# Performance work log

Measured on AMD Instinct MI355X. Metric: run time of the kernel, lower is better.

The kernel has to match this reference:

```python
import jax, jax.numpy as jnp
import numpy as np

N_NODES = 50000
N_EDGES = 800000
IN_DIM = 4
HID = 64
N_LAYERS = 3
BN_EPS = 1e-5


def setup_inputs() -> dict:
    key = jax.random.key(0)
    ks = jax.random.split(key, 16)
    x = jax.random.normal(ks[0], (N_NODES, IN_DIM), dtype=jnp.float32)
    edge_index = jax.random.randint(ks[1], (2, N_EDGES), 0, N_NODES, dtype=jnp.int32)
    # input projection
    W_in = jax.random.normal(ks[2], (IN_DIM, HID), dtype=jnp.float32) * 0.1
    b_in = jnp.zeros((HID,), dtype=jnp.float32)
    # stacked per-layer GCN weights and BatchNorm (eval-mode) params
    conv_w = jax.random.normal(ks[3], (N_LAYERS, HID, HID), dtype=jnp.float32) * 0.1
    conv_b = jnp.zeros((N_LAYERS, HID), dtype=jnp.float32)
    bn_gamma = jnp.ones((N_LAYERS, HID), dtype=jnp.float32)
    bn_beta = jnp.zeros((N_LAYERS, HID), dtype=jnp.float32)
    bn_mean = jax.random.normal(ks[4], (N_LAYERS, HID), dtype=jnp.float32) * 0.01
    bn_var = jnp.abs(jax.random.normal(ks[5], (N_LAYERS, HID), dtype=jnp.float32)) * 0.1 + 1.0
    # output projection: Linear(HID,HID) -> ReLU -> Dropout(eval: identity) -> Linear(HID,OUT)
    W1 = jax.random.normal(ks[6], (HID, HID), dtype=jnp.float32) * 0.1
    b1 = jnp.zeros((HID,), dtype=jnp.float32)
    W2 = jax.random.normal(ks[7], (HID, IN_DIM), dtype=jnp.float32) * 0.01  # xavier gain 0.1
    b2 = jnp.zeros((IN_DIM,), dtype=jnp.float32)
    return {
        "x": x, "edge_index": edge_index,
        "W_in": W_in, "b_in": b_in,
        "conv_w": conv_w, "conv_b": conv_b,
        "bn_gamma": bn_gamma, "bn_beta": bn_beta,
        "bn_mean": bn_mean, "bn_var": bn_var,
        "W1": W1, "b1": b1, "W2": W2, "b2": b2,
    }


def _gcn_graph(edge_index, n_nodes):
    """Add self loops and compute symmetric GCN normalization per edge."""
    loops = jnp.arange(n_nodes, dtype=edge_index.dtype)
    src = jnp.concatenate([edge_index[0], loops])
    dst = jnp.concatenate([edge_index[1], loops])
    deg = jax.ops.segment_sum(jnp.ones_like(dst, dtype=jnp.float32), dst,
                              num_segments=n_nodes)  # in-degree incl. self loop
    dinv = jax.lax.rsqrt(jnp.maximum(deg, 1e-12))
    enorm = dinv[src] * dinv[dst]  # [E+N]
    return src, dst, enorm


def reference(x, edge_index, W_in, b_in, conv_w, conv_b, bn_gamma, bn_beta,
              bn_mean, bn_var, W1, b1, W2, b2):
    n = x.shape[0]
    src, dst, enorm = _gcn_graph(edge_index, n)

    input_x = x
    h = x @ W_in + b_in  # [N, HID]
    for i in range(N_LAYERS):
        residual = h
        # GCNConv: linear -> normalized gather/scatter aggregate -> bias
        hw = h @ conv_w[i]
        msg = hw[src] * enorm[:, None]  # [E+N, HID] irregular gather
        h = jax.ops.segment_sum(msg, dst, num_segments=n) + conv_b[i]
        # BatchNorm1d (eval) + ReLU (dropout is identity in eval)
        h = (h - bn_mean[i]) * jax.lax.rsqrt(bn_var[i] + BN_EPS) * bn_gamma[i] + bn_beta[i]
        h = jax.nn.relu(h)
        h = h + residual  # shapes always match (HID == HID)
    # output projection MLP
    delta = jax.nn.relu(h @ W1 + b1) @ W2 + b2  # [N, IN_DIM]
    return input_x + delta
```

## Files before the change

### kernel.cpp

```cpp
#include <hip/hip_runtime.h>

#define HID 64
#define CAP 64

__device__ __forceinline__ float bf2f(unsigned short u) {
    return __uint_as_float(((unsigned)u) << 16);
}
__device__ __forceinline__ unsigned short f2bf(float f) {
    unsigned u = __float_as_uint(f);
    u += 0x7FFF + ((u >> 16) & 1);
    return (unsigned short)(u >> 16);
}

__global__ void fill_gemm(const int* __restrict__ eidx, int* __restrict__ cursor,
                          int* __restrict__ col, int E, int n, int nodes_per,
                          int chunk, int fillBlocks,
                          const float* __restrict__ x, const float* __restrict__ Win,
                          const float* __restrict__ bin, const float* __restrict__ W,
                          float* __restrict__ h, unsigned short* __restrict__ hws0) {
    if (blockIdx.x < fillBlocks) {
        int p = blockIdx.x & 7;
        int q = blockIdx.x >> 3;
        const int* __restrict__ dst = eidx + E;
        int lo = p * nodes_per;
        int hi = lo + nodes_per;
        int beg = q * chunk;
        int end = min(beg + chunk, E);
        int vend = beg + ((end - beg) & ~3);
        for (int e = beg + threadIdx.x * 4; e < vend; e += 1024) {
            int4 dv = *(const int4*)&dst[e];
            if (dv.x >= lo && dv.x < hi) {
                int s = eidx[e];
                int pos = atomicAdd(&cursor[dv.x], 1);
                if (pos < CAP) col[(dv.x << 6) + pos] = s;
            }
            if (dv.y >= lo && dv.y < hi) {
                int s = eidx[e + 1];
                int pos = atomicAdd(&cursor[dv.y], 1);
                if (pos < CAP) col[(dv.y << 6) + pos] = s;
            }
            if (dv.z >= lo && dv.z < hi) {
                int s = eidx[e + 2];
                int pos = atomicAdd(&cursor[dv.z], 1);
                if (pos < CAP) col[(dv.z << 6) + pos] = s;
            }
            if (dv.w >= lo && dv.w < hi) {
                int s = eidx[e + 3];
                int pos = atomicAdd(&cursor[dv.w], 1);
                if (pos < CAP) col[(dv.w << 6) + pos] = s;
            }
        }
        for (int e = vend + threadIdx.x; e < end; e += 256) {
            int d = dst[e];
            if (d >= lo && d < hi) {
                int s = eidx[e];
                int pos = atomicAdd(&cursor[d], 1);
                if (pos < CAP) col[(d << 6) + pos] = s;
            }
        }
        return;
    }
    __shared__ float wl[64 * 64];
    __shared__ float winl[256];
    __shared__ float binl[64];
    __shared__ float hl[256];
    int b = blockIdx.x - fillBlocks;
    int tid = threadIdx.x;
#pragma unroll
    for (int i = 0; i < 16; ++i) wl[tid + 256 * i] = W[tid + 256 * i];
    winl[tid] = Win[tid];
    if (tid < 64) binl[tid] = bin[tid];
    int j = tid & 63;
    int w = tid >> 6;
    for (int c = 0; c < 8; ++c) {
        int v = b * 32 + c * 4 + w;
        __syncthreads();
        float hv = 0.f;
        if (v < n) {
            float4 xv = *(const float4*)&x[(size_t)v * 4];
            hv = binl[j] + xv.x * winl[j] + xv.y * winl[64 + j]
                         + xv.z * winl[128 + j] + xv.w * winl[192 + j];
            h[(size_t)v * 64 + j] = hv;
        }
        hl[tid] = hv;
        __syncthreads();
        if (v < n) {
            const float* hr = &hl[w * 64];
            float acc = 0.f;
#pragma unroll
            for (int k = 0; k < 64; ++k) acc += hr[k] * wl[k * 64 + j];
            hws0[(size_t)v * 64 + j] = f2bf(acc);
        }
    }
}

#define GATHER_BODY(hws4, col, cursor, beg, end, s0, s1, s2, s3, gl)              \
    {                                                                             \
        int e = beg;                                                              \
        for (; e + 7 < end; e += 8) {                                             \
            int c0 = col[e], c1 = col[e+1], c2 = col[e+2], c3 = col[e+3];         \
            int c4 = col[e+4], c5 = col[e+5], c6 = col[e+6], c7 = col[e+7];       \
            float d0 = rsqrtf((float)cursor[c0] + 1.0f);                          \
            float d1 = rsqrtf((float)cursor[c1] + 1.0f);                          \
            float d2 = rsqrtf((float)cursor[c2] + 1.0f);                          \
            float d3 = rsqrtf((float)cursor[c3] + 1.0f);                          \
            float d4 = rsqrtf((float)cursor[c4] + 1.0f);                          \
            float d5 = rsqrtf((float)cursor[c5] + 1.0f);                          \
            float d6 = rsqrtf((float)cursor[c6] + 1.0f);                          \
            float d7 = rsqrtf((float)cursor[c7] + 1.0f);                          \
            ushort4 m0 = hws4[(size_t)c0 * 16 + gl];                              \
            ushort4 m1 = hws4[(size_t)c1 * 16 + gl];                              \
            ushort4 m2 = hws4[(size_t)c2 * 16 + gl];                              \
            ushort4 m3 = hws4[(size_t)c3 * 16 + gl];                              \
            ushort4 m4 = hws4[(size_t)c4 * 16 + gl];                              \
            ushort4 m5 = hws4[(size_t)c5 * 16 + gl];                              \
            ushort4 m6 = hws4[(size_t)c6 * 16 + gl];                              \
            ushort4 m7 = hws4[(size_t)c7 * 16 + gl];                              \
            s0 = fmaf(bf2f(m0.x), d0, s0); s0 = fmaf(bf2f(m1.x), d1, s0);         \
            s0 = fmaf(bf2f(m2.x), d2, s0); s0 = fmaf(bf2f(m3.x), d3, s0);         \
            s0 = fmaf(bf2f(m4.x), d4, s0); s0 = fmaf(bf2f(m5.x), d5, s0);         \
            s0 = fmaf(bf2f(m6.x), d6, s0); s0 = fmaf(bf2f(m7.x), d7, s0);         \
            s1 = fmaf(bf2f(m0.y), d0, s1); s1 = fmaf(bf2f(m1.y), d1, s1);         \
            s1 = fmaf(bf2f(m2.y), d2, s1); s1 = fmaf(bf2f(m3.y), d3, s1);         \
            s1 = fmaf(bf2f(m4.y), d4, s1); s1 = fmaf(bf2f(m5.y), d5, s1);         \
            s1 = fmaf(bf2f(m6.y), d6, s1); s1 = fmaf(bf2f(m7.y), d7, s1);         \
            s2 = fmaf(bf2f(m0.z), d0, s2); s2 = fmaf(bf2f(m1.z), d1, s2);         \
            s2 = fmaf(bf2f(m2.z), d2, s2); s2 = fmaf(bf2f(m3.z), d3, s2);         \
            s2 = fmaf(bf2f(m4.z), d4, s2); s2 = fmaf(bf2f(m5.z), d5, s2);         \
            s2 = fmaf(bf2f(m6.z), d6, s2); s2 = fmaf(bf2f(m7.z), d7, s2);         \
            s3 = fmaf(bf2f(m0.w), d0, s3); s3 = fmaf(bf2f(m1.w), d1, s3);         \
            s3 = fmaf(bf2f(m2.w), d2, s3); s3 = fmaf(bf2f(m3.w), d3, s3);         \
            s3 = fmaf(bf2f(m4.w), d4, s3); s3 = fmaf(bf2f(m5.w), d5, s3);         \
            s3 = fmaf(bf2f(m6.w), d6, s3); s3 = fmaf(bf2f(m7.w), d7, s3);         \
        }                                                                         \
        for (; e + 3 < end; e += 4) {                                             \
            int c0 = col[e], c1 = col[e+1], c2 = col[e+2], c3 = col[e+3];         \
            float d0 = rsqrtf((float)cursor[c0] + 1.0f);                          \
            float d1 = rsqrtf((float)cursor[c1] + 1.0f);                          \
            float d2 = rsqrtf((float)cursor[c2] + 1.0f);                          \
            float d3 = rsqrtf((float)cursor[c3] + 1.0f);                          \
            ushort4 m0 = hws4[(size_t)c0 * 16 + gl];                              \
            ushort4 m1 = hws4[(size_t)c1 * 16 + gl];                              \
            ushort4 m2 = hws4[(size_t)c2 * 16 + gl];                              \
            ushort4 m3 = hws4[(size_t)c3 * 16 + gl];                              \
            s0 = fmaf(bf2f(m0.x), d0, s0); s0 = fmaf(bf2f(m1.x), d1, s0);         \
            s0 = fmaf(bf2f(m2.x), d2, s0); s0 = fmaf(bf2f(m3.x), d3, s0);         \
            s1 = fmaf(bf2f(m0.y), d0, s1); s1 = fmaf(bf2f(m1.y), d1, s1);         \
            s1 = fmaf(bf2f(m2.y), d2, s1); s1 = fmaf(bf2f(m3.y), d3, s1);         \
            s2 = fmaf(bf2f(m0.z), d0, s2); s2 = fmaf(bf2f(m1.z), d1, s2);         \
            s2 = fmaf(bf2f(m2.z), d2, s2); s2 = fmaf(bf2f(m3.z), d3, s2);         \
            s3 = fmaf(bf2f(m0.w), d0, s3); s3 = fmaf(bf2f(m1.w), d1, s3);         \
            s3 = fmaf(bf2f(m2.w), d2, s3); s3 = fmaf(bf2f(m3.w), d3, s3);         \
        }                                                                         \
        for (; e < end; ++e) {                                                    \
            int c0 = col[e];                                                      \
            float d0 = rsqrtf((float)cursor[c0] + 1.0f);                          \
            ushort4 me = hws4[(size_t)c0 * 16 + gl];                              \
            s0 = fmaf(bf2f(me.x), d0, s0); s1 = fmaf(bf2f(me.y), d0, s1);         \
            s2 = fmaf(bf2f(me.z), d0, s2); s3 = fmaf(bf2f(me.w), d0, s3);         \
        }                                                                         \
    }

__global__ void gather_gemm(const int* __restrict__ cursor, const int* __restrict__ col,
                            const unsigned short* __restrict__ hws_in,
                            float* __restrict__ h,
                            const float* __restrict__ cb, const float* __restrict__ gamma,
                            const float* __restrict__ beta, const float* __restrict__ mean,
                            const float* __restrict__ var, const float* __restrict__ Wn,
                            unsigned short* __restrict__ hws_out, int n) {
    __shared__ float wl[64 * 64];
    __shared__ float hl[16 * 64];
    int tid = threadIdx.x;
#pragma unroll
    for (int i = 0; i < 16; ++i) wl[tid + 256 * i] = Wn[tid + 256 * i];
    int lane = tid & 63, wave = tid >> 6;
    int grp = lane >> 4, gl = lane & 15;
    int ln = wave * 4 + grp;
    int v = blockIdx.x * 16 + ln;
    bool valid = v < n;
    int vv = valid ? v : 0;
    int j0 = gl * 4;
    const ushort4* hws4 = (const ushort4*)hws_in;
    int cnt = cursor[vv];
    float di = rsqrtf((float)cnt + 1.0f);
    ushort4 m = hws4[(size_t)vv * 16 + gl];
    float s0 = bf2f(m.x) * di, s1 = bf2f(m.y) * di,
          s2 = bf2f(m.z) * di, s3 = bf2f(m.w) * di;
    int beg = vv << 6;
    int end = beg + (valid ? min(cnt, CAP) : 0);
    GATHER_BODY(hws4, col, cursor, beg, end, s0, s1, s2, s3, gl)
    float4 cbv = *(const float4*)&cb[j0];
    float4 mnv = *(const float4*)&mean[j0];
    float4 vrv = *(const float4*)&var[j0];
    float4 gmv = *(const float4*)&gamma[j0];
    float4 btv = *(const float4*)&beta[j0];
    float4 hres = *(const float4*)&h[(size_t)vv * 64 + j0];
    float4 o;
    o.x = fmaxf((s0 * di + cbv.x - mnv.x) * rsqrtf(vrv.x + 1e-5f) * gmv.x + btv.x, 0.f) + hres.x;
    o.y = fmaxf((s1 * di + cbv.y - mnv.y) * rsqrtf(vrv.y + 1e-5f) * gmv.y + btv.y, 0.f) + hres.y;
    o.z = fmaxf((s2 * di + cbv.z - mnv.z) * rsqrtf(vrv.z + 1e-5f) * gmv.z + btv.z, 0.f) + hres.z;
    o.w = fmaxf((s3 * di + cbv.w - mnv.w) * rsqrtf(vrv.w + 1e-5f) * gmv.w + btv.w, 0.f) + hres.w;
    if (valid) *(float4*)&h[(size_t)vv * 64 + j0] = o;
    *(float4*)&hl[ln * 64 + j0] = o;
    __syncthreads();
    int j = lane;
    for (int c = 0; c < 4; ++c) {
        int ln2 = wave * 4 + c;
        int v2 = blockIdx.x * 16 + ln2;
        if (v2 < n) {
            const float* hr = &hl[ln2 * 64];
            float acc = 0.f;
#pragma unroll
            for (int k = 0; k < 64; ++k) acc += hr[k] * wl[k * 64 + j];
            hws_out[(size_t)v2 * 64 + j] = f2bf(acc);
        }
    }
}

__global__ void gather_mlp(const int* __restrict__ cursor, const int* __restrict__ col,
                           const unsigned short* __restrict__ hws_in,
                           const float* __restrict__ h,
                           const float* __restrict__ cb, const float* __restrict__ gamma,
                           const float* __restrict__ beta, const float* __restrict__ mean,
                           const float* __restrict__ var, const float* __restrict__ x,
                           const float* __restrict__ W1, const float* __restrict__ b1,
                           const float* __restrict__ W2, const float* __restrict__ b2,
                           float* __restrict__ out, int n) {
    __shared__ float wl[64 * 64];
    __shared__ float w2l[256];
    __shared__ float hl[16 * 64];
    __shared__ float tl[16 * 68];
    int tid = threadIdx.x;
#pragma unroll
    for (int i = 0; i < 16; ++i) wl[tid + 256 * i] = W1[tid + 256 * i];
    w2l[tid] = W2[tid];
    int lane = tid & 63, wave = tid >> 6;
    int grp = lane >> 4, gl = lane & 15;
    int ln = wave * 4 + grp;
    int v = blockIdx.x * 16 + ln;
    bool valid = v < n;
    int vv = valid ? v : 0;
    int j0 = gl * 4;
    const ushort4* hws4 = (const ushort4*)hws_in;
    int cnt = cursor[vv];
    float di = rsqrtf((float)cnt + 1.0f);
    ushort4 m = hws4[(size_t)vv * 16 + gl];
    float s0 = bf2f(m.x) * di, s1 = bf2f(m.y) * di,
          s2 = bf2f(m.z) * di, s3 = bf2f(m.w) * di;
    int beg = vv << 6;
    int end = beg + (valid ? min(cnt, CAP) : 0);
    GATHER_BODY(hws4, col, cursor, beg, end, s0, s1, s2, s3, gl)
    float4 cbv = *(const float4*)&cb[j0];
    float4 mnv = *(const float4*)&mean[j0];
    float4 vrv = *(const float4*)&var[j0];
    float4 gmv = *(const float4*)&gamma[j0];
    float4 btv = *(const float4*)&beta[j0];
    float4 hres = *(const float4*)&h[(size_t)vv * 64 + j0];
    float4 o;
    o.x = fmaxf((s0 * di + cbv.x - mnv.x) * rsqrtf(vrv.x + 1e-5f) * gmv.x + btv.x, 0.f) + hres.x;
    o.y = fmaxf((s1 * di + cbv.y - mnv.y) * rsqrtf(vrv.y + 1e-5f) * gmv.y + btv.y, 0.f) + hres.y;
    o.z = fmaxf((s2 * di + cbv.z - mnv.z) * rsqrtf(vrv.z + 1e-5f) * gmv.z + btv.z, 0.f) + hres.z;
    o.w = fmaxf((s3 * di + cbv.w - mnv.w) * rsqrtf(vrv.w + 1e-5f) * gmv.w + btv.w, 0.f) + hres.w;
    *(float4*)&hl[ln * 64 + j0] = o;
    __syncthreads();
    int j = lane;
    float b1j = b1[j];
    for (int c = 0; c < 4; ++c) {
        int ln2 = wave * 4 + c;
        const float* hr = &hl[ln2 * 64];
        float acc = b1j;
#pragma unroll
        for (int k = 0; k < 64; ++k) acc += hr[k] * wl[k * 64 + j];
        tl[ln2 * 68 + j] = fmaxf(acc, 0.f);
    }
    __syncthreads();
    if (tid < 64) {
        int ln2 = tid >> 2, mm = tid & 3;
        int v2 = blockIdx.x * 16 + ln2;
        if (v2 < n) {
            const float* tr = &tl[ln2 * 68];
            float acc = b2[mm];
#pragma unroll
            for (int k = 0; k < 64; ++k) acc += tr[k] * w2l[k * 4 + mm];
            out[(size_t)v2 * 4 + mm] = x[(size_t)v2 * 4 + mm] + acc;
        }
    }
}

extern "C" void kernel_launch(void* const* d_in, const int* in_sizes, int n_in,
                              void* d_out, int out_size, void* d_ws, size_t ws_size,
                              hipStream_t stream) {
    const float* x     = (const float*)d_in[0];
    const int*   eidx  = (const int*)  d_in[1];
    const float* Win   = (const float*)d_in[2];
    const float* bin   = (const float*)d_in[3];
    const float* convw = (const float*)d_in[4];
    const float* convb = (const float*)d_in[5];
    const float* gamma = (const float*)d_in[6];
    const float* beta  = (const float*)d_in[7];
    const float* mean  = (const float*)d_in[8];
    const float* var   = (const float*)d_in[9];
    const float* W1    = (const float*)d_in[10];
    const float* b1    = (const float*)d_in[11];
    const float* W2    = (const float*)d_in[12];
    const float* b2    = (const float*)d_in[13];
    float* out = (float*)d_out;

    int n = in_sizes[0] / 4;
    int E = in_sizes[1] / 2;
    const int B = 256;

    char* p = (char*)d_ws;
    size_t nh = (size_t)n * 64;
    float*          h      = (float*)p;          p += nh * 4;
    unsigned short* hws0   = (unsigned short*)p; p += nh * 2;
    unsigned short* hws1   = (unsigned short*)p; p += nh * 2;
    int*            cursor = (int*)p;            p += ((size_t)n + 16) * 4;
    int*            col    = (int*)p;            p += (size_t)n * CAP * 4;

    const int GP = 128;
    int fillBlocks = GP * 8;
    int nodes_per = (n + 7) / 8;
    int chunk = (((E + GP - 1) / GP) + 3) & ~3;

    hipMemsetAsync(cursor, 0, (size_t)n * 4, stream);
    int NB32 = (n + 31) / 32;
    fill_gemm<<<fillBlocks + NB32, B, 0, stream>>>(
        eidx, cursor, col, E, n, nodes_per, chunk, fillBlocks,
        x, Win, bin, convw, h, hws0);

    int NB16 = (n + 15) / 16;
    gather_gemm<<<NB16, B, 0, stream>>>(cursor, col, hws0, h,
        convb, gamma, beta, mean, var, convw + 4096, hws1, n);
    gather_gemm<<<NB16, B, 0, stream>>>(cursor, col, hws1, h,
        convb + 64, gamma + 64, beta + 64, mean + 64, var + 64, convw + 8192, hws0, n);
    gather_mlp<<<NB16, B, 0, stream>>>(cursor, col, hws0, h,
        convb + 128, gamma + 128, beta + 128, mean + 128, var + 128,
        x, W1, b1, W2, b2, out, n);
}
```

Baseline: 233.2 us.

## Partition each node's neighbor list by source half using packed dual counters

The per-node cursor now packs two 16-bit counters, one for sources below n/2 and one for sources above. Low-half sources are stored from the front of the 64-slot list and high-half sources from the back. The gather then runs two passes, low-index sources first and high-index sources second, aiming for better cache locality on the irregular hws reads. This adds a second loop with its own remainder handling and extra decode ALU, and the degree is now capped per half rather than overall.

```diff
diff --git a/kernel.cpp b/kernel.cpp
--- a/kernel.cpp
+++ b/kernel.cpp
@@ -12,8 +12,10 @@
     return (unsigned short)(u >> 16);
 }
 
-__global__ void fill_gemm(const int* __restrict__ eidx, int* __restrict__ cursor,
-                          int* __restrict__ col, int E, int n, int nodes_per,
+#define DINV(cc) rsqrtf((float)(((cc) & 0xffffu) + ((cc) >> 16)) + 1.0f)
+
+__global__ void fill_gemm(const int* __restrict__ eidx, unsigned* __restrict__ cursor,
+                          int* __restrict__ col, int E, int n, int mid, int nodes_per,
                           int chunk, int fillBlocks,
                           const float* __restrict__ x, const float* __restrict__ Win,
                           const float* __restrict__ bin, const float* __restrict__ W,
@@ -29,34 +31,23 @@
         int vend = beg + ((end - beg) & ~3);
         for (int e = beg + threadIdx.x * 4; e < vend; e += 1024) {
             int4 dv = *(const int4*)&dst[e];
-            if (dv.x >= lo && dv.x < hi) {
-                int s = eidx[e];
-                int pos = atomicAdd(&cursor[dv.x], 1);
-                if (pos < CAP) col[(dv.x << 6) + pos] = s;
+#define FILL_ONE(d, ei)                                                        \
+            if (d >= lo && d < hi) {                                           \
+                int s = eidx[ei];                                              \
+                bool low = s < mid;                                            \
+                unsigned old = atomicAdd(&cursor[d], low ? 1u : 0x10000u);     \
+                unsigned cp = low ? (old & 0xffffu) : (old >> 16);             \
+                if (cp < CAP) col[(d << 6) + (low ? cp : (CAP - 1u - cp))] = s;\
             }
-            if (dv.y >= lo && dv.y < hi) {
-                int s = eidx[e + 1];
-                int pos = atomicAdd(&cursor[dv.y], 1);
-                if (pos < CAP) col[(dv.y << 6) + pos] = s;
-            }
-            if (dv.z >= lo && dv.z < hi) {
-                int s = eidx[e + 2];
-                int pos = atomicAdd(&cursor[dv.z], 1);
-                if (pos < CAP) col[(dv.z << 6) + pos] = s;
-            }
-            if (dv.w >= lo && dv.w < hi) {
-                int s = eidx[e + 3];
-                int pos = atomicAdd(&cursor[dv.w], 1);
-                if (pos < CAP) col[(dv.w << 6) + pos] = s;
-            }
+            FILL_ONE(dv.x, e)
+            FILL_ONE(dv.y, e + 1)
+            FILL_ONE(dv.z, e + 2)
+            FILL_ONE(dv.w, e + 3)
         }
         for (int e = vend + threadIdx.x; e < end; e += 256) {
             int d = dst[e];
-            if (d >= lo && d < hi) {
-                int s = eidx[e];
-                int pos = atomicAdd(&cursor[d], 1);
-                if (pos < CAP) col[(d << 6) + pos] = s;
-            }
+            FILL_ONE(d, e)
+#undef FILL_ONE
         }
         return;
     }
@@ -94,20 +85,16 @@
     }
 }
 
-#define GATHER_BODY(hws4, col, cursor, beg, end, s0, s1, s2, s3, gl)              \
+#define GATHER_BODY(hws4, col, cur, beg, end, s0, s1, s2, s3, gl)                 \
     {                                                                             \
         int e = beg;                                                              \
         for (; e + 7 < end; e += 8) {                                             \
             int c0 = col[e], c1 = col[e+1], c2 = col[e+2], c3 = col[e+3];         \
             int c4 = col[e+4], c5 = col[e+5], c6 = col[e+6], c7 = col[e+7];       \
-            float d0 = rsqrtf((float)cursor[c0] + 1.0f);                          \
-            float d1 = rsqrtf((float)cursor[c1] + 1.0f);                          \
-            float d2 = rsqrtf((float)cursor[c2] + 1.0f);                          \
-            float d3 = rsqrtf((float)cursor[c3] + 1.0f);                          \
-            float d4 = rsqrtf((float)cursor[c4] + 1.0f);                          \
-            float d5 = rsqrtf((float)cursor[c5] + 1.0f);                          \
-            float d6 = rsqrtf((float)cursor[c6] + 1.0f);                          \
-            float d7 = rsqrtf((float)cursor[c7] + 1.0f);                          \
+            unsigned k0 = cur[c0], k1 = cur[c1], k2 = cur[c2], k3 = cur[c3];      \
+            unsigned k4 = cur[c4], k5 = cur[c5], k6 = cur[c6], k7 = cur[c7];      \
+            float d0 = DINV(k0), d1 = DINV(k1), d2 = DINV(k2), d3 = DINV(k3);     \
+            float d4 = DINV(k4), d5 = DINV(k5), d6 = DINV(k6), d7 = DINV(k7);     \
             ushort4 m0 = hws4[(size_t)c0 * 16 + gl];                              \
             ushort4 m1 = hws4[(size_t)c1 * 16 + gl];                              \
             ushort4 m2 = hws4[(size_t)c2 * 16 + gl];                              \
@@ -135,10 +122,8 @@
         }                                                                         \
         for (; e + 3 < end; e += 4) {                                             \
             int c0 = col[e], c1 = col[e+1], c2 = col[e+2], c3 = col[e+3];         \
-            float d0 = rsqrtf((float)cursor[c0] + 1.0f);                          \
-            float d1 = rsqrtf((float)cursor[c1] + 1.0f);                          \
-            float d2 = rsqrtf((float)cursor[c2] + 1.0f);                          \
-            float d3 = rsqrtf((float)cursor[c3] + 1.0f);                          \
+            unsigned k0 = cur[c0], k1 = cur[c1], k2 = cur[c2], k3 = cur[c3];      \
+            float d0 = DINV(k0), d1 = DINV(k1), d2 = DINV(k2), d3 = DINV(k3);     \
             ushort4 m0 = hws4[(size_t)c0 * 16 + gl];                              \
             ushort4 m1 = hws4[(size_t)c1 * 16 + gl];                              \
             ushort4 m2 = hws4[(size_t)c2 * 16 + gl];                              \
@@ -154,14 +139,15 @@
         }                                                                         \
         for (; e < end; ++e) {                                                    \
             int c0 = col[e];                                                      \
-            float d0 = rsqrtf((float)cursor[c0] + 1.0f);                          \
+            unsigned k0 = cur[c0];                                                \
+            float d0 = DINV(k0);                                                  \
             ushort4 me = hws4[(size_t)c0 * 16 + gl];                              \
             s0 = fmaf(bf2f(me.x), d0, s0); s1 = fmaf(bf2f(me.y), d0, s1);         \
             s2 = fmaf(bf2f(me.z), d0, s2); s3 = fmaf(bf2f(me.w), d0, s3);         \
         }                                                                         \
     }
 
-__global__ void gather_gemm(const int* __restrict__ cursor, const int* __restrict__ col,
+__global__ void gather_gemm(const unsigned* __restrict__ cursor, const int* __restrict__ col,
                             const unsigned short* __restrict__ hws_in,
                             float* __restrict__ h,
                             const float* __restrict__ cb, const float* __restrict__ gamma,
@@ -181,14 +167,17 @@
     int vv = valid ? v : 0;
     int j0 = gl * 4;
     const ushort4* hws4 = (const ushort4*)hws_in;
-    int cnt = cursor[vv];
-    float di = rsqrtf((float)cnt + 1.0f);
+    unsigned cc = cursor[vv];
+    int nlo = cc & 0xffffu, nhi = cc >> 16;
+    float di = rsqrtf((float)(nlo + nhi) + 1.0f);
     ushort4 m = hws4[(size_t)vv * 16 + gl];
     float s0 = bf2f(m.x) * di, s1 = bf2f(m.y) * di,
           s2 = bf2f(m.z) * di, s3 = bf2f(m.w) * di;
-    int beg = vv << 6;
-    int end = beg + (valid ? min(cnt, CAP) : 0);
-    GATHER_BODY(hws4, col, cursor, beg, end, s0, s1, s2, s3, gl)
+    int base = vv << 6;
+    int nlo_c = valid ? min(nlo, CAP) : 0;
+    int nhi_c = valid ? min(nhi, CAP) : 0;
+    GATHER_BODY(hws4, col, cursor, base, base + nlo_c, s0, s1, s2, s3, gl)
+    GATHER_BODY(hws4, col, cursor, base + CAP - nhi_c, base + CAP, s0, s1, s2, s3, gl)
     float4 cbv = *(const float4*)&cb[j0];
     float4 mnv = *(const float4*)&mean[j0];
     float4 vrv = *(const float4*)&var[j0];
@@ -217,7 +206,7 @@
     }
 }
 
-__global__ void gather_mlp(const int* __restrict__ cursor, const int* __restrict__ col,
+__global__ void gather_mlp(const unsigned* __restrict__ cursor, const int* __restrict__ col,
                            const unsigned short* __restrict__ hws_in,
                            const float* __restrict__ h,
                            const float* __restrict__ cb, const float* __restrict__ gamma,
@@ -242,14 +231,17 @@
     int vv = valid ? v : 0;
     int j0 = gl * 4;
     const ushort4* hws4 = (const ushort4*)hws_in;
-    int cnt = cursor[vv];
-    float di = rsqrtf((float)cnt + 1.0f);
+    unsigned cc = cursor[vv];
+    int nlo = cc & 0xffffu, nhi = cc >> 16;
+    float di = rsqrtf((float)(nlo + nhi) + 1.0f);
     ushort4 m = hws4[(size_t)vv * 16 + gl];
     float s0 = bf2f(m.x) * di, s1 = bf2f(m.y) * di,
           s2 = bf2f(m.z) * di, s3 = bf2f(m.w) * di;
-    int beg = vv << 6;
-    int end = beg + (valid ? min(cnt, CAP) : 0);
-    GATHER_BODY(hws4, col, cursor, beg, end, s0, s1, s2, s3, gl)
+    int base = vv << 6;
+    int nlo_c = valid ? min(nlo, CAP) : 0;
+    int nhi_c = valid ? min(nhi, CAP) : 0;
+    GATHER_BODY(hws4, col, cursor, base, base + nlo_c, s0, s1, s2, s3, gl)
+    GATHER_BODY(hws4, col, cursor, base + CAP - nhi_c, base + CAP, s0, s1, s2, s3, gl)
     float4 cbv = *(const float4*)&cb[j0];
     float4 mnv = *(const float4*)&mean[j0];
     float4 vrv = *(const float4*)&var[j0];
@@ -315,18 +307,19 @@
     float*          h      = (float*)p;          p += nh * 4;
     unsigned short* hws0   = (unsigned short*)p; p += nh * 2;
     unsigned short* hws1   = (unsigned short*)p; p += nh * 2;
-    int*            cursor = (int*)p;            p += ((size_t)n + 16) * 4;
+    unsigned*       cursor = (unsigned*)p;       p += ((size_t)n + 16) * 4;
     int*            col    = (int*)p;            p += (size_t)n * CAP * 4;
 
     const int GP = 128;
     int fillBlocks = GP * 8;
     int nodes_per = (n + 7) / 8;
     int chunk = (((E + GP - 1) / GP) + 3) & ~3;
+    int mid = n >> 1;
 
     hipMemsetAsync(cursor, 0, (size_t)n * 4, stream);
     int NB32 = (n + 31) / 32;
     fill_gemm<<<fillBlocks + NB32, B, 0, stream>>>(
-        eidx, cursor, col, E, n, nodes_per, chunk, fillBlocks,
+        eidx, cursor, col, E, n, mid, nodes_per, chunk, fillBlocks,
         x, Win, bin, convw, h, hws0);
 
     int NB16 = (n + 15) / 16;
```

Measured after the change: 250.9 us. +7.6%, slower.

## Prescale GCN features by source degree and widen gather to 8 bf16 per lane

Applied to the files above, without the earlier changes.

The GEMM epilogues of the first two gather kernels now multiply each output row by its own rsqrt(deg), so later layers can sum neighbour rows without looking up each neighbour's degree. This removes a dependent cursor load and an rsqrt per edge in layers two and three. Each lane now loads 8 bf16 values (16 bytes), and a block handles 32 nodes instead of 16. The cost is more shared memory per block and more registers per thread, which may lower occupancy, and the first layer still uses the per-edge degree path because fill_gemm writes unscaled features.

```diff
diff --git a/kernel.cpp b/kernel.cpp
--- a/kernel.cpp
+++ b/kernel.cpp
@@ -1,7 +1,8 @@
 #include <hip/hip_runtime.h>
 
-#define HID 64
 #define CAP 64
+
+typedef unsigned short us8 __attribute__((ext_vector_type(8)));
 
 __device__ __forceinline__ float bf2f(unsigned short u) {
     return __uint_as_float(((unsigned)u) << 16);
@@ -94,73 +95,60 @@
     }
 }
 
-#define GATHER_BODY(hws4, col, cursor, beg, end, s0, s1, s2, s3, gl)              \
+#define GH_D8(hwsp, col, cur, beg, end, s, gl8)                                   \
     {                                                                             \
         int e = beg;                                                              \
         for (; e + 7 < end; e += 8) {                                             \
-            int c0 = col[e], c1 = col[e+1], c2 = col[e+2], c3 = col[e+3];         \
-            int c4 = col[e+4], c5 = col[e+5], c6 = col[e+6], c7 = col[e+7];       \
-            float d0 = rsqrtf((float)cursor[c0] + 1.0f);                          \
-            float d1 = rsqrtf((float)cursor[c1] + 1.0f);                          \
-            float d2 = rsqrtf((float)cursor[c2] + 1.0f);                          \
-            float d3 = rsqrtf((float)cursor[c3] + 1.0f);                          \
-            float d4 = rsqrtf((float)cursor[c4] + 1.0f);                          \
-            float d5 = rsqrtf((float)cursor[c5] + 1.0f);                          \
-            float d6 = rsqrtf((float)cursor[c6] + 1.0f);                          \
-            float d7 = rsqrtf((float)cursor[c7] + 1.0f);                          \
-            ushort4 m0 = hws4[(size_t)c0 * 16 + gl];                              \
-            ushort4 m1 = hws4[(size_t)c1 * 16 + gl];                              \
-            ushort4 m2 = hws4[(size_t)c2 * 16 + gl];                              \
-            ushort4 m3 = hws4[(size_t)c3 * 16 + gl];                              \
-            ushort4 m4 = hws4[(size_t)c4 * 16 + gl];                              \
-            ushort4 m5 = hws4[(size_t)c5 * 16 + gl];                              \
-            ushort4 m6 = hws4[(size_t)c6 * 16 + gl];                              \
-            ushort4 m7 = hws4[(size_t)c7 * 16 + gl];                              \
-            s0 = fmaf(bf2f(m0.x), d0, s0); s0 = fmaf(bf2f(m1.x), d1, s0);         \
-            s0 = fmaf(bf2f(m2.x), d2, s0); s0 = fmaf(bf2f(m3.x), d3, s0);         \
-            s0 = fmaf(bf2f(m4.x), d4, s0); s0 = fmaf(bf2f(m5.x), d5, s0);         \
-            s0 = fmaf(bf2f(m6.x), d6, s0); s0 = fmaf(bf2f(m7.x), d7, s0);         \
-            s1 = fmaf(bf2f(m0.y), d0, s1); s1 = fmaf(bf2f(m1.y), d1, s1);         \
-            s1 = fmaf(bf2f(m2.y), d2, s1); s1 = fmaf(bf2f(m3.y), d3, s1);         \
-            s1 = fmaf(bf2f(m4.y), d4, s1); s1 = fmaf(bf2f(m5.y), d5, s1);         \
-            s1 = fmaf(bf2f(m6.y), d6, s1); s1 = fmaf(bf2f(m7.y), d7, s1);         \
-            s2 = fmaf(bf2f(m0.z), d0, s2); s2 = fmaf(bf2f(m1.z), d1, s2);         \
-            s2 = fmaf(bf2f(m2.z), d2, s2); s2 = fmaf(bf2f(m3.z), d3, s2);         \
-            s2 = fmaf(bf2f(m4.z), d4, s2); s2 = fmaf(bf2f(m5.z), d5, s2);         \
-            s2 = fmaf(bf2f(m6.z), d6, s2); s2 = fmaf(bf2f(m7.z), d7, s2);         \
-            s3 = fmaf(bf2f(m0.w), d0, s3); s3 = fmaf(bf2f(m1.w), d1, s3);         \
-            s3 = fmaf(bf2f(m2.w), d2, s3); s3 = fmaf(bf2f(m3.w), d3, s3);         \
-            s3 = fmaf(bf2f(m4.w), d4, s3); s3 = fmaf(bf2f(m5.w), d5, s3);         \
-            s3 = fmaf(bf2f(m6.w), d6, s3); s3 = fmaf(bf2f(m7.w), d7, s3);         \
-        }                                                                         \
-        for (; e + 3 < end; e += 4) {                                             \
-            int c0 = col[e], c1 = col[e+1], c2 = col[e+2], c3 = col[e+3];         \
-            float d0 = rsqrtf((float)cursor[c0] + 1.0f);                          \
-            float d1 = rsqrtf((float)cursor[c1] + 1.0f);                          \
-            float d2 = rsqrtf((float)cursor[c2] + 1.0f);                          \
-            float d3 = rsqrtf((float)cursor[c3] + 1.0f);                          \
-            ushort4 m0 = hws4[(size_t)c0 * 16 + gl];                              \
-            ushort4 m1 = hws4[(size_t)c1 * 16 + gl];                              \
-            ushort4 m2 = hws4[(size_t)c2 * 16 + gl];                              \
-            ushort4 m3 = hws4[(size_t)c3 * 16 + gl];                              \
-            s0 = fmaf(bf2f(m0.x), d0, s0); s0 = fmaf(bf2f(m1.x), d1, s0);         \
-            s0 = fmaf(bf2f(m2.x), d2, s0); s0 = fmaf(bf2f(m3.x), d3, s0);         \
-            s1 = fmaf(bf2f(m0.y), d0, s1); s1 = fmaf(bf2f(m1.y), d1, s1);         \
-            s1 = fmaf(bf2f(m2.y), d2, s1); s1 = fmaf(bf2f(m3.y), d3, s1);         \
-            s2 = fmaf(bf2f(m0.z), d0, s2); s2 = fmaf(bf2f(m1.z), d1, s2);         \
-            s2 = fmaf(bf2f(m2.z), d2, s2); s2 = fmaf(bf2f(m3.z), d3, s2);         \
-            s3 = fmaf(bf2f(m0.w), d0, s3); s3 = fmaf(bf2f(m1.w), d1, s3);         \
-            s3 = fmaf(bf2f(m2.w), d2, s3); s3 = fmaf(bf2f(m3.w), d3, s3);         \
+            int cc[8]; float dd[8]; us8 mm[8];                                    \
+            _Pragma("unroll")                                                     \
+            for (int i = 0; i < 8; ++i) cc[i] = col[e + i];                       \
+            _Pragma("unroll")                                                     \
+            for (int i = 0; i < 8; ++i)                                           \
+                mm[i] = *(const us8*)&hwsp[(size_t)cc[i] * 64 + (gl8) * 8];       \
+            _Pragma("unroll")                                                     \
+            for (int i = 0; i < 8; ++i)                                           \
+                dd[i] = rsqrtf((float)cur[cc[i]] + 1.0f);                         \
+            _Pragma("unroll")                                                     \
+            for (int i = 0; i < 8; ++i) {                                         \
+                _Pragma("unroll")                                                 \
+                for (int f = 0; f < 8; ++f)                                       \
+                    s[f] = fmaf(bf2f(mm[i][f]), dd[i], s[f]);                     \
+            }                                                                     \
         }                                                                         \
         for (; e < end; ++e) {                                                    \
             int c0 = col[e];                                                      \
-            float d0 = rsqrtf((float)cursor[c0] + 1.0f);                          \
-            ushort4 me = hws4[(size_t)c0 * 16 + gl];                              \
-            s0 = fmaf(bf2f(me.x), d0, s0); s1 = fmaf(bf2f(me.y), d0, s1);         \
-            s2 = fmaf(bf2f(me.z), d0, s2); s3 = fmaf(bf2f(me.w), d0, s3);         \
+            float d0 = rsqrtf((float)cur[c0] + 1.0f);                             \
+            us8 me = *(const us8*)&hwsp[(size_t)c0 * 64 + (gl8) * 8];             \
+            _Pragma("unroll")                                                     \
+            for (int f = 0; f < 8; ++f)                                           \
+                s[f] = fmaf(bf2f(me[f]), d0, s[f]);                               \
         }                                                                         \
     }
 
+#define GH_P8(hwsp, col, beg, end, s, gl8)                                        \
+    {                                                                             \
+        int e = beg;                                                              \
+        for (; e + 7 < end; e += 8) {                                             \
+            int cc[8]; us8 mm[8];                                                 \
+            _Pragma("unroll")                                                     \
+            for (int i = 0; i < 8; ++i) cc[i] = col[e + i];                       \
+            _Pragma("unroll")                                                     \
+            for (int i = 0; i < 8; ++i)                                           \
+                mm[i] = *(const us8*)&hwsp[(size_t)cc[i] * 64 + (gl8) * 8];       \
+            _Pragma("unroll")                                                     \
+            for (int f = 0; f < 8; ++f)                                           \
+                s[f] += bf2f(mm[0][f]) + bf2f(mm[1][f]) + bf2f(mm[2][f])          \
+                      + bf2f(mm[3][f]) + bf2f(mm[4][f]) + bf2f(mm[5][f])          \
+                      + bf2f(mm[6][f]) + bf2f(mm[7][f]);                          \
+        }                                                                         \
+        for (; e < end; ++e) {                                                    \
+            us8 me = *(const us8*)&hwsp[(size_t)col[e] * 64 + (gl8) * 8];         \
+            _Pragma("unroll")                                                     \
+            for (int f = 0; f < 8; ++f) s[f] += bf2f(me[f]);                      \
+        }                                                                         \
+    }
+
+template <bool PRESCALED>
 __global__ void gather_gemm(const int* __restrict__ cursor, const int* __restrict__ col,
                             const unsigned short* __restrict__ hws_in,
                             float* __restrict__ h,
@@ -169,50 +157,62 @@
                             const float* __restrict__ var, const float* __restrict__ Wn,
                             unsigned short* __restrict__ hws_out, int n) {
     __shared__ float wl[64 * 64];
-    __shared__ float hl[16 * 64];
+    __shared__ float hl[32 * 64];
     int tid = threadIdx.x;
 #pragma unroll
     for (int i = 0; i < 16; ++i) wl[tid + 256 * i] = Wn[tid + 256 * i];
     int lane = tid & 63, wave = tid >> 6;
-    int grp = lane >> 4, gl = lane & 15;
-    int ln = wave * 4 + grp;
-    int v = blockIdx.x * 16 + ln;
+    int grp8 = lane >> 3, gl8 = lane & 7;
+    int ln = wave * 8 + grp8;
+    int v = blockIdx.x * 32 + ln;
     bool valid = v < n;
     int vv = valid ? v : 0;
-    int j0 = gl * 4;
-    const ushort4* hws4 = (const ushort4*)hws_in;
     int cnt = cursor[vv];
     float di = rsqrtf((float)cnt + 1.0f);
-    ushort4 m = hws4[(size_t)vv * 16 + gl];
-    float s0 = bf2f(m.x) * di, s1 = bf2f(m.y) * di,
-          s2 = bf2f(m.z) * di, s3 = bf2f(m.w) * di;
+    us8 m = *(const us8*)&hws_in[(size_t)vv * 64 + gl8 * 8];
+    float s[8];
+#pragma unroll
+    for (int f = 0; f < 8; ++f) s[f] = PRESCALED ? bf2f(m[f]) : bf2f(m[f]) * di;
     int beg = vv << 6;
     int end = beg + (valid ? min(cnt, CAP) : 0);
-    GATHER_BODY(hws4, col, cursor, beg, end, s0, s1, s2, s3, gl)
-    float4 cbv = *(const float4*)&cb[j0];
-    float4 mnv = *(const float4*)&mean[j0];
-    float4 vrv = *(const float4*)&var[j0];
-    float4 gmv = *(const float4*)&gamma[j0];
-    float4 btv = *(const float4*)&beta[j0];
-    float4 hres = *(const float4*)&h[(size_t)vv * 64 + j0];
-    float4 o;
-    o.x = fmaxf((s0 * di + cbv.x - mnv.x) * rsqrtf(vrv.x + 1e-5f) * gmv.x + btv.x, 0.f) + hres.x;
-    o.y = fmaxf((s1 * di + cbv.y - mnv.y) * rsqrtf(vrv.y + 1e-5f) * gmv.y + btv.y, 0.f) + hres.y;
-    o.z = fmaxf((s2 * di + cbv.z - mnv.z) * rsqrtf(vrv.z + 1e-5f) * gmv.z + btv.z, 0.f) + hres.z;
-    o.w = fmaxf((s3 * di + cbv.w - mnv.w) * rsqrtf(vrv.w + 1e-5f) * gmv.w + btv.w, 0.f) + hres.w;
-    if (valid) *(float4*)&h[(size_t)vv * 64 + j0] = o;
-    *(float4*)&hl[ln * 64 + j0] = o;
+    if (PRESCALED) {
+        GH_P8(hws_in, col, beg, end, s, gl8)
+    } else {
+        GH_D8(hws_in, col, cursor, beg, end, s, gl8)
+    }
+    int j0 = gl8 * 8;
+    float o[8];
+#pragma unroll
+    for (int hf = 0; hf < 2; ++hf) {
+        int jb = j0 + hf * 4;
+        float4 cbv = *(const float4*)&cb[jb];
+        float4 mnv = *(const float4*)&mean[jb];
+        float4 vrv = *(const float4*)&var[jb];
+        float4 gmv = *(const float4*)&gamma[jb];
+        float4 btv = *(const float4*)&beta[jb];
+        float4 hres = *(const float4*)&h[(size_t)vv * 64 + jb];
+        float4 oo;
+        oo.x = fmaxf((s[hf*4+0] * di + cbv.x - mnv.x) * rsqrtf(vrv.x + 1e-5f) * gmv.x + btv.x, 0.f) + hres.x;
+        oo.y = fmaxf((s[hf*4+1] * di + cbv.y - mnv.y) * rsqrtf(vrv.y + 1e-5f) * gmv.y + btv.y, 0.f) + hres.y;
+        oo.z = fmaxf((s[hf*4+2] * di + cbv.z - mnv.z) * rsqrtf(vrv.z + 1e-5f) * gmv.z + btv.z, 0.f) + hres.z;
+        oo.w = fmaxf((s[hf*4+3] * di + cbv.w - mnv.w) * rsqrtf(vrv.w + 1e-5f) * gmv.w + btv.w, 0.f) + hres.w;
+        if (valid) *(float4*)&h[(size_t)vv * 64 + jb] = oo;
+        *(float4*)&hl[ln * 64 + jb] = oo;
+        o[hf*4+0] = oo.x; o[hf*4+1] = oo.y; o[hf*4+2] = oo.z; o[hf*4+3] = oo.w;
+    }
+    (void)o;
     __syncthreads();
     int j = lane;
-    for (int c = 0; c < 4; ++c) {
-        int ln2 = wave * 4 + c;
-        int v2 = blockIdx.x * 16 + ln2;
+    for (int c = 0; c < 8; ++c) {
+        int ln2 = wave * 8 + c;
+        int v2 = blockIdx.x * 32 + ln2;
         if (v2 < n) {
             const float* hr = &hl[ln2 * 64];
             float acc = 0.f;
 #pragma unroll
             for (int k = 0; k < 64; ++k) acc += hr[k] * wl[k * 64 + j];
-            hws_out[(size_t)v2 * 64 + j] = f2bf(acc);
+            float di2 = rsqrtf((float)cursor[v2] + 1.0f);
+            hws_out[(size_t)v2 * 64 + j] = f2bf(acc * di2);
         }
     }
 }
@@ -228,45 +228,49 @@
                            float* __restrict__ out, int n) {
     __shared__ float wl[64 * 64];
     __shared__ float w2l[256];
-    __shared__ float hl[16 * 64];
-    __shared__ float tl[16 * 68];
+    __shared__ float hl[32 * 64];
+    __shared__ float tl[32 * 68];
     int tid = threadIdx.x;
 #pragma unroll
     for (int i = 0; i < 16; ++i) wl[tid + 256 * i] = W1[tid + 256 * i];
     w2l[tid] = W2[tid];
     int lane = tid & 63, wave = tid >> 6;
-    int grp = lane >> 4, gl = lane & 15;
-    int ln = wave * 4 + grp;
-    int v = blockIdx.x * 16 + ln;
+    int grp8 = lane >> 3, gl8 = lane & 7;
+    int ln = wave * 8 + grp8;
+    int v = blockIdx.x * 32 + ln;
     bool valid = v < n;
     int vv = valid ? v : 0;
-    int j0 = gl * 4;
-    const ushort4* hws4 = (const ushort4*)hws_in;
     int cnt = cursor[vv];
     float di = rsqrtf((float)cnt + 1.0f);
-    ushort4 m = hws4[(size_t)vv * 16 + gl];
-    float s0 = bf2f(m.x) * di, s1 = bf2f(m.y) * di,
-          s2 = bf2f(m.z) * di, s3 = bf2f(m.w) * di;
+    us8 m = *(const us8*)&hws_in[(size_t)vv * 64 + gl8 * 8];
+    float s[8];
+#pragma unroll
+    for (int f = 0; f < 8; ++f) s[f] = bf2f(m[f]);
     int beg = vv << 6;
     int end = beg + (valid ? min(cnt, CAP) : 0);
-    GATHER_BODY(hws4, col, cursor, beg, end, s0, s1, s2, s3, gl)
-    float4 cbv = *(const float4*)&cb[j0];
-    float4 mnv = *(const float4*)&mean[j0];
-    float4 vrv = *(const float4*)&var[j0];
-    float4 gmv = *(const float4*)&gamma[j0];
-    float4 btv = *(const float4*)&beta[j0];
-    float4 hres = *(const float4*)&h[(size_t)vv * 64 + j0];
-    float4 o;
-    o.x = fmaxf((s0 * di + cbv.x - mnv.x) * rsqrtf(vrv.x + 1e-5f) * gmv.x + btv.x, 0.f) + hres.x;
-    o.y = fmaxf((s1 * di + cbv.y - mnv.y) * rsqrtf(vrv.y + 1e-5f) * gmv.y + btv.y, 0.f) + hres.y;
-    o.z = fmaxf((s2 * di + cbv.z - mnv.z) * rsqrtf(vrv.z + 1e-5f) * gmv.z + btv.z, 0.f) + hres.z;
-    o.w = fmaxf((s3 * di + cbv.w - mnv.w) * rsqrtf(vrv.w + 1e-5f) * gmv.w + btv.w, 0.f) + hres.w;
-    *(float4*)&hl[ln * 64 + j0] = o;
+    GH_P8(hws_in, col, beg, end, s, gl8)
+    int j0 = gl8 * 8;
+#pragma unroll
+    for (int hf = 0; hf < 2; ++hf) {
+        int jb = j0 + hf * 4;
+        float4 cbv = *(const float4*)&cb[jb];
+        float4 mnv = *(const float4*)&mean[jb];
+        float4 vrv = *(const float4*)&var[jb];
+        float4 gmv = *(const float4*)&gamma[jb];
+        float4 btv = *(const float4*)&beta[jb];
+        float4 hres = *(const float4*)&h[(size_t)vv * 64 + jb];
+        float4 oo;
+        oo.x = fmaxf((s[hf*4+0] * di + cbv.x - mnv.x) * rsqrtf(vrv.x + 1e-5f) * gmv.x + btv.x, 0.f) + hres.x;
+        oo.y = fmaxf((s[hf*4+1] * di + cbv.y - mnv.y) * rsqrtf(vrv.y + 1e-5f) * gmv.y + btv.y, 0.f) + hres.y;
+        oo.z = fmaxf((s[hf*4+2] * di + cbv.z - mnv.z) * rsqrtf(vrv.z + 1e-5f) * gmv.z + btv.z, 0.f) + hres.z;
+        oo.w = fmaxf((s[hf*4+3] * di + cbv.w - mnv.w) * rsqrtf(vrv.w + 1e-5f) * gmv.w + btv.w, 0.f) + hres.w;
+        *(float4*)&hl[ln * 64 + jb] = oo;
+    }
     __syncthreads();
     int j = lane;
     float b1j = b1[j];
-    for (int c = 0; c < 4; ++c) {
-        int ln2 = wave * 4 + c;
+    for (int c = 0; c < 8; ++c) {
+        int ln2 = wave * 8 + c;
         const float* hr = &hl[ln2 * 64];
         float acc = b1j;
 #pragma unroll
@@ -274,9 +278,9 @@
         tl[ln2 * 68 + j] = fmaxf(acc, 0.f);
     }
     __syncthreads();
-    if (tid < 64) {
+    if (tid < 128) {
         int ln2 = tid >> 2, mm = tid & 3;
-        int v2 = blockIdx.x * 16 + ln2;
+        int v2 = blockIdx.x * 32 + ln2;
         if (v2 < n) {
             const float* tr = &tl[ln2 * 68];
             float acc = b2[mm];
@@ -329,12 +333,12 @@
         eidx, cursor, col, E, n, nodes_per, chunk, fillBlocks,
         x, Win, bin, convw, h, hws0);
 
-    int NB16 = (n + 15) / 16;
-    gather_gemm<<<NB16, B, 0, stream>>>(cursor, col, hws0, h,
+    int NB32g = (n + 31) / 32;
+    gather_gemm<false><<<NB32g, B, 0, stream>>>(cursor, col, hws0, h,
         convb, gamma, beta, mean, var, convw + 4096, hws1, n);
-    gather_gemm<<<NB16, B, 0, stream>>>(cursor, col, hws1, h,
+    gather_gemm<true><<<NB32g, B, 0, stream>>>(cursor, col, hws1, h,
         convb + 64, gamma + 64, beta + 64, mean + 64, var + 64, convw + 8192, hws0, n);
-    gather_mlp<<<NB16, B, 0, stream>>>(cursor, col, hws0, h,
+    gather_mlp<<<NB32g, B, 0, stream>>>(cursor, col, hws0, h,
         convb + 128, gamma + 128, beta + 128, mean + 128, var + 128,
         x, W1, b1, W2, b2, out, n);
 }
```

New measurement: 233.4 us. No clear change (+0.1%).
